# Kernel tuning notes

Measured on AMD Instinct MI355X. Metric: run time of the kernel, lower is better.

Reference implementation:

```python
import jax, jax.numpy as jnp
import numpy as np

LOCAL_SIZE = 128
LN_EPS = 1e-5


def _ln(x):
    # F.layer_norm over last axis, no affine params
    mu = jnp.mean(x, axis=-1, keepdims=True)
    var = jnp.var(x, axis=-1, keepdims=True)
    return (x - mu) / jnp.sqrt(var + LN_EPS)


def _rel_shift(x):
    # x: [b, n, qlen, klen] -> Transformer-XL relative shift
    b, n, q, k = x.shape
    xp = jnp.pad(x, ((0, 0), (0, 0), (0, 0), (1, 0)))
    xp = xp.reshape(b, n, k + 1, q)
    return xp[:, :, 1:, :].reshape(b, n, q, k)


def setup_inputs() -> dict:
    key = jax.random.key(0)
    ks = jax.random.split(key, 12)
    bsz, d_model, qlen, mlen = 16, 1024, 256, 256
    n_head, d_head, d_inner = 16, 64, 4096
    klen = qlen + mlen
    s = 0.02  # param init scale
    return {
        "z1ss": jax.random.normal(ks[0], (bsz, d_model, qlen), jnp.float32),
        "uss": jax.random.normal(ks[1], (bsz, 3 * n_head * d_head, klen), jnp.float32) * 0.1,
        "mems": jax.random.normal(ks[2], (bsz, d_model, mlen), jnp.float32),
        "pos_emb": jax.random.normal(ks[3], (d_model, klen), jnp.float32),
        "Wqkv": jax.random.normal(ks[4], (3 * n_head * d_head, d_model), jnp.float32) * s,
        "Wr": jax.random.normal(ks[5], (n_head * d_head, d_model), jnp.float32) * s,
        "Wo": jax.random.normal(ks[6], (d_model, n_head * d_head), jnp.float32) * s,
        "bo": jnp.zeros((d_model,), jnp.float32),
        "r_w_bias": jax.random.uniform(ks[7], (n_head, d_head), jnp.float32, -0.05, 0.05),
        "r_r_bias": jax.random.uniform(ks[8], (n_head, d_head), jnp.float32, -0.05, 0.05),
        "W1": jax.random.normal(ks[9], (d_inner, d_model), jnp.float32) * s,
        "b1": jnp.zeros((d_inner,), jnp.float32),
        "W2": jax.random.normal(ks[10], (d_model, d_inner), jnp.float32) * s,
        "b2": jnp.zeros((d_model,), jnp.float32),
    }


def reference(z1ss, uss, mems, pos_emb, Wqkv, Wr, Wo, bo, r_w_bias, r_r_bias, W1, b1, W2, b2):
    bsz, d_model, qlen = z1ss.shape
    mlen = mems.shape[-1]
    n_head, d_head = r_w_bias.shape
    scale = 1.0 / (d_head ** 0.5)

    # ---- self-attention with relative positions ----
    cat = jnp.concatenate([mems, z1ss], axis=-1)            # [b, d, klen]
    klen = cat.shape[-1]
    w_heads = jnp.einsum('od,bdk->bok', Wqkv, cat) + uss     # [b, 3*n*dh, klen]
    r_head_k = (Wr @ pos_emb).reshape(n_head, d_head, -1)    # [n, dh, rlen]

    q, k, v = jnp.split(w_heads, 3, axis=1)
    q = q[:, :, -qlen:].reshape(bsz, n_head, d_head, qlen)   # [b, n, dh, q]
    k = k.reshape(bsz, n_head, d_head, klen)
    v = v.reshape(bsz, n_head, d_head, klen)

    AC = jnp.einsum('bndi,bndj->bnij', q + r_w_bias[:, :, None], k)
    BD = jnp.einsum('bndi,ndj->bnij', q + r_r_bias[:, :, None], r_head_k)
    BD = _rel_shift(BD)
    attn_score = (AC + BD) * scale                            # [b, n, q, klen]

    # causal + local-window mask
    i = jnp.arange(qlen)[:, None]
    j = jnp.arange(klen)[None, :]
    mask = (j > i + mlen) | (j <= i + mlen - LOCAL_SIZE)      # [q, klen]
    attn_score = jnp.where(mask[None, None], -1e30, attn_score)

    attn_prob = jax.nn.softmax(attn_score, axis=-1)
    attn_vec = jnp.einsum('bnij,bndj->bndi', attn_prob, v)    # [b, n, dh, q]
    attn_vec = attn_vec.reshape(bsz, n_head * d_head, qlen)
    attn_out = jnp.einsum('od,bdq->boq', Wo, attn_vec) + bo[None, :, None]

    # post-LN residual (pre_lnorm=False), work in [b, q, d]
    h = _ln((attn_out + z1ss).transpose(0, 2, 1))             # [b, q, d]

    # ---- position-wise FF ----
    ff = jax.nn.relu(jnp.einsum('bqd,id->bqi', h, W1) + b1)
    ff = jnp.einsum('bqi,di->bqd', ff, W2) + b2
    out = _ln(ff + h)                                          # [b, q, d]
    return out.transpose(0, 2, 1)                              # [b, d, q]
```

## Files before the change

### kernel.cpp

```cpp
#include <hip/hip_runtime.h>
#include <hip/hip_bf16.h>
#include <math.h>

#define BSZ    16
#define DMODEL 1024
#define QLEN   256
#define MLEN   256
#define KLEN   512
#define NHEAD  16
#define DHEAD  64
#define DINNER 4096

typedef __bf16 bf16;
typedef bf16 bf16x8 __attribute__((ext_vector_type(8)));
typedef float f32x4 __attribute__((ext_vector_type(4)));

#define GLOBAL_AS __attribute__((address_space(1)))
#define LDS_AS    __attribute__((address_space(3)))

__global__ __launch_bounds__(256) void prep_k(
    const float* __restrict__ Wqkv, const float* __restrict__ Wr,
    const float* __restrict__ Wo,   const float* __restrict__ W1,
    const float* __restrict__ W2,   const float* __restrict__ uss,
    const float* __restrict__ mems, const float* __restrict__ z1ss,
    const float* __restrict__ pos_emb,
    bf16* __restrict__ WqkvB, bf16* __restrict__ WrB, bf16* __restrict__ WoB,
    bf16* __restrict__ W1B,   bf16* __restrict__ W2B, bf16* __restrict__ ussV,
    bf16* __restrict__ catT,  bf16* __restrict__ posT,
    bf16* __restrict__ ussQ,  bf16* __restrict__ ussK)
{
    if (blockIdx.x < 21504) {
        long long i = (long long)blockIdx.x * 256 + threadIdx.x;
        const float* src; bf16* dst; long long soff, doff;
        if      (i <  786432) { src = Wqkv; dst = WqkvB; soff = doff = i; }
        else if (i < 1048576) { src = Wr;   dst = WrB;   soff = doff = i -  786432; }
        else if (i < 1310720) { src = Wo;   dst = WoB;   soff = doff = i - 1048576; }
        else if (i < 2359296) { src = W1;   dst = W1B;   soff = doff = i - 1310720; }
        else if (i < 3407872) { src = W2;   dst = W2B;   soff = doff = i - 2359296; }
        else {
            long long u = i - 3407872, b = u >> 17, r = u & 131071;
            src = uss; dst = ussV; soff = b * 393216 + 262144 + r; doff = u;
        }
        float4 v = ((const float4*)src)[soff];
        bf16 b0 = (bf16)v.x, b1 = (bf16)v.y, b2 = (bf16)v.z, b3 = (bf16)v.w;
        union { ushort u[4]; uint2 d; } p;
        p.u[0] = *(ushort*)&b0; p.u[1] = *(ushort*)&b1;
        p.u[2] = *(ushort*)&b2; p.u[3] = *(ushort*)&b3;
        ((uint2*)dst)[doff] = p.d;
        return;
    }
    __shared__ float tile[32][33];
    int blk = blockIdx.x - 21504;
    const float* src; bf16* dst; long long soff, dof; int ld, ldo, tr, tc;
    if (blk < 8192) {
        int bh = blk >> 8, t = blk & 255;
        int b = bh >> 1, half = bh & 1;
        tr = t >> 3; tc = t & 7;
        src = half ? z1ss : mems; soff = (long long)b * 1024 * 256; ld = 256;
        dst = catT; dof = ((long long)b * 512 + half * 256) * 1024; ldo = 1024;
    } else if (blk < 8704) {
        int u = blk - 8192; tr = u >> 4; tc = u & 15;
        src = pos_emb; soff = 0; ld = 512;
        dst = posT; dof = 0; ldo = 1024;
    } else if (blk < 12800) {
        int u = blk - 8704; int b = u >> 8, t = u & 255;
        tr = t >> 3; tc = t & 7;
        src = uss; soff = (long long)b * 3072 * 512 + 256; ld = 512;
        dst = ussQ; dof = (long long)b * 256 * 1024; ldo = 1024;
    } else {
        int u = blk - 12800; int b = u >> 9, t = u & 511;
        tr = t >> 4; tc = t & 15;
        src = uss; soff = ((long long)b * 3072 + 1024) * 512; ld = 512;
        dst = ussK; dof = (long long)b * 512 * 1024; ldo = 1024;
    }
    int tx = threadIdx.x & 31, ty = threadIdx.x >> 5;
    const float* ip = src + soff;
#pragma unroll
    for (int yy = ty; yy < 32; yy += 8)
        tile[yy][tx] = ip[(long long)(tr * 32 + yy) * ld + tc * 32 + tx];
    __syncthreads();
#pragma unroll
    for (int yy = ty; yy < 32; yy += 8)
        dst[dof + (long long)(tc * 32 + yy) * ldo + tr * 32 + tx] = (bf16)tile[tx][yy];
}


__device__ __forceinline__ void stage_a_unit(const bf16* __restrict__ Ag, int ldK,
                                             bf16* sAbuf, int qa, int t) {
    int r  = (t >> 2) & 63;
    int ks = t >> 8;
    int cc = (t & 3) ^ (((t >> 5) & 1) << 1);
    int col = ks * 32 + cc * 8;
    __builtin_amdgcn_global_load_lds(
        (const GLOBAL_AS void*)(Ag + (long long)(qa * 64 + r) * ldK + col),
        (LDS_AS void*)(sAbuf + qa * 4096 + t * 8), 16, 0, 0);
    __builtin_amdgcn_global_load_lds(
        (const GLOBAL_AS void*)(Ag + (long long)(qa * 64 + 128 + r) * ldK + col),
        (LDS_AS void*)(sAbuf + (qa + 2) * 4096 + t * 8), 16, 0, 0);
}

__device__ __forceinline__ void stage_b_unit(const bf16* __restrict__ Bg, int ldK,
                                             bf16* sBbuf, int qb, int t) {
#pragma unroll
    for (int j = 0; j < 2; ++j) {
        int u  = j * 512 + t;
        int p  = u >> 8;
        int w8 = u & 255;
        int ks = w8 >> 7;
        int r  = (w8 >> 2) & 31;
        int cc = (u & 3) ^ (((t >> 5) & 1) << 1);
        __builtin_amdgcn_global_load_lds(
            (const GLOBAL_AS void*)(Bg + (long long)(p * 64 + qb * 32 + r) * ldK + ks * 32 + cc * 8),
            (LDS_AS void*)(sBbuf + p * 4096 + ks * 2048 + qb * 1024 + r * 32 + (u & 3) * 8),
            16, 0, 0);
    }
}

__device__ __forceinline__ void ld_a(const bf16* sAbuf, int qa, int wm, int lane,
                                     bf16x8 a[4][2]) {
    int r16 = lane & 15, qq = lane >> 4;
    int flip = ((r16 >> 3) & 1) << 4;
    const bf16* base = sAbuf + (wm * 2 + qa) * 4096;
#pragma unroll
    for (int mf = 0; mf < 4; ++mf)
#pragma unroll
        for (int ks = 0; ks < 2; ++ks)
            a[mf][ks] = *(const bf16x8*)(base +
                ((ks * 2048 + (mf * 16 + r16) * 32 + qq * 8) ^ flip));
}

__device__ __forceinline__ void ld_b(const bf16* sBbuf, int qb, int wn, int lane,
                                     bf16x8 b[2][2]) {
    int r16 = lane & 15, qq = lane >> 4;
    int flip = ((r16 >> 3) & 1) << 4;
    const bf16* base = sBbuf + wn * 4096 + qb * 1024;
#pragma unroll
    for (int nf = 0; nf < 2; ++nf)
#pragma unroll
        for (int ks = 0; ks < 2; ++ks)
            b[nf][ks] = *(const bf16x8*)(base +
                ((ks * 2048 + (nf * 16 + r16) * 32 + qq * 8) ^ flip));
}

#define PH_SYNC_MFMA(QA, QB)                                                   \
    __builtin_amdgcn_s_barrier();                                              \
    asm volatile("s_waitcnt lgkmcnt(0)" ::: "memory");                         \
    __builtin_amdgcn_s_setprio(1);                                             \
    _Pragma("unroll") for (int ks = 0; ks < 2; ++ks)                           \
    _Pragma("unroll") for (int mf = 0; mf < 4; ++mf)                           \
    _Pragma("unroll") for (int nf = 0; nf < 2; ++nf)                           \
        acc[(QA)*4+mf][(QB)*2+nf] = __builtin_amdgcn_mfma_f32_16x16x32_bf16(   \
            a[mf][ks], b[nf][ks], acc[(QA)*4+mf][(QB)*2+nf], 0, 0, 0);         \
    __builtin_amdgcn_s_setprio(0);                                             \
    __builtin_amdgcn_s_barrier();

__device__ __forceinline__ void gemm8_core(
    const bf16* __restrict__ Ap, const bf16* __restrict__ Bp,
    int ldK, int NT, bf16* sA, bf16* sB, f32x4 (&acc)[8][4])
{
    int t = threadIdx.x;
    int lane = t & 63, w = t >> 6;
    int wm = w >> 2, wn = w & 3;

    stage_a_unit(Ap, ldK, sA, 0, t);
    stage_a_unit(Ap, ldK, sA, 1, t);
    stage_b_unit(Bp, ldK, sB, 0, t);
    stage_b_unit(Bp, ldK, sB, 1, t);
    stage_b_unit(Bp + 64, ldK, sB + 16384, 0, t);
    stage_a_unit(Ap + 64, ldK, sA + 16384, 1, t);
    stage_b_unit(Bp + 64, ldK, sB + 16384, 1, t);
    asm volatile("s_waitcnt vmcnt(6)" ::: "memory");
    __builtin_amdgcn_s_barrier();

    bf16x8 a[4][2], b[2][2];
    for (int g = 0; g < NT; ++g) {
        bf16* AR = sA + (g & 1) * 16384;
        bf16* BR = sB + (g & 1) * 16384;
        bf16* AO = sA + ((g & 1) ^ 1) * 16384;
        const bf16* An = Ap + (long long)(g + 1) * 64;
        const bf16* A2 = Ap + (long long)(g + 2) * 64;
        const bf16* B2 = Bp + (long long)(g + 2) * 64;
        ld_a(AR, 0, wm, lane, a);
        ld_b(BR, 0, wn, lane, b);
        if (g + 1 < NT) stage_a_unit(An, ldK, AO, 0, t);
        PH_SYNC_MFMA(0, 0)
        ld_a(AR, 1, wm, lane, a);
        if (g + 2 < NT) stage_b_unit(B2, ldK, BR, 0, t);
        PH_SYNC_MFMA(1, 0)
        ld_b(BR, 1, wn, lane, b);
        if (g + 2 < NT) stage_a_unit(A2, ldK, AR, 1, t);
        PH_SYNC_MFMA(1, 1)
        ld_a(AR, 0, wm, lane, a);
        if (g + 2 < NT) stage_b_unit(B2, ldK, BR, 1, t);
        if (g < NT - 2) asm volatile("s_waitcnt vmcnt(6)" ::: "memory");
        else            asm volatile("s_waitcnt vmcnt(0)" ::: "memory");
        PH_SYNC_MFMA(0, 1)
    }
}

__global__ __launch_bounds__(512) void qkv8_k(
    const bf16* __restrict__ catT, const bf16* __restrict__ WqkvB,
    const bf16* __restrict__ posT, const bf16* __restrict__ WrB,
    const bf16* __restrict__ ussQ, const bf16* __restrict__ ussK,
    const bf16* __restrict__ ussV,
    bf16* __restrict__ qT, bf16* __restrict__ kT,
    bf16* __restrict__ rhkT, bf16* __restrict__ vB)
{
    __shared__ bf16 sm[65536];
    int f = blockIdx.x;
    int id = (f & 7) * 41 + (f >> 3);

    const bf16 *Ap, *Bp;
    bf16* outp; const bf16* addp;
    long long obase; int ostr;
    if (id < 320) {
        int b = id / 20, rb = id % 20;
        const bf16* cat = catT + (long long)b * 524288;
        if (rb < 4) {
            int n0 = rb << 8;
            Ap = cat + 256 * 1024; Bp = WqkvB + (long long)n0 * 1024;
            outp = qT; addp = ussQ;
            obase = ((long long)b * 256) * 1024 + n0; ostr = 1024;
        } else if (rb < 12) {
            int rr = rb - 4, m0 = (rr >> 2) << 8, n0 = (rr & 3) << 8;
            Ap = cat + (long long)m0 * 1024; Bp = WqkvB + (long long)(1024 + n0) * 1024;
            outp = kT; addp = ussK;
            obase = ((long long)(b * 512 + m0)) * 1024 + n0; ostr = 1024;
        } else {
            int rr = rb - 12, m0 = (rr >> 1) << 8, n0 = (rr & 1) << 8;
            Ap = WqkvB + (long long)(2048 + m0) * 1024; Bp = cat + (long long)n0 * 1024;
            outp = vB; addp = ussV;
            obase = ((long long)(b * 1024 + m0)) * 512 + n0; ostr = 512;
        }
    } else {
        int r = id - 320, m0 = (r >> 2) << 8, n0 = (r & 3) << 8;
        Ap = posT + (long long)m0 * 1024; Bp = WrB + (long long)n0 * 1024;
        outp = rhkT; addp = nullptr;
        obase = (long long)m0 * 1024 + n0; ostr = 1024;
    }

    f32x4 acc[8][4];
#pragma unroll
    for (int i = 0; i < 8; ++i)
#pragma unroll
        for (int j = 0; j < 4; ++j) acc[i][j] = (f32x4){0.f, 0.f, 0.f, 0.f};

    gemm8_core(Ap, Bp, 1024, 16, sm, sm + 32768, acc);

    int t = threadIdx.x, lane = t & 63, w = t >> 6;
    int wm = w >> 2, wn = w & 3;
    int qq = lane >> 4, r16 = lane & 15;
#pragma unroll
    for (int mf = 0; mf < 8; ++mf) {
#pragma unroll
        for (int rr2 = 0; rr2 < 4; ++rr2) {
            int ml = wm * 128 + mf * 16 + qq * 4 + rr2;
#pragma unroll
            for (int nf = 0; nf < 4; ++nf) {
                int nl = wn * 64 + nf * 16 + r16;
                long long idx = obase + (long long)ml * ostr + nl;
                float v = acc[mf][nf][rr2];
                if (addp) v += (float)addp[idx];
                outp[idx] = (bf16)v;
            }
        }
    }
}

__global__ __launch_bounds__(512) void gemm8_k(
    const bf16* __restrict__ A, const bf16* __restrict__ B,
    int N, int K,
    const float* __restrict__ bias, int relu,
    bf16* __restrict__ outB)
{
    __shared__ bf16 sm[65536];
    int nwg = gridDim.x, f = blockIdx.x;
    int xcd = f & 7, l = f >> 3;
    int q8 = nwg >> 3, rm = nwg & 7;
    int wg = (xcd < rm) ? (xcd * (q8 + 1) + l)
                        : (rm * (q8 + 1) + (xcd - rm) * q8 + l);
    int ntn = N >> 8;
    int m0 = (wg / ntn) << 8, n0 = (wg % ntn) << 8;

    f32x4 acc[8][4];
#pragma unroll
    for (int i = 0; i < 8; ++i)
#pragma unroll
        for (int j = 0; j < 4; ++j) acc[i][j] = (f32x4){0.f, 0.f, 0.f, 0.f};

    gemm8_core(A + (long long)m0 * K, B + (long long)n0 * K, K, K >> 6,
               sm, sm + 32768, acc);

    int t = threadIdx.x, lane = t & 63, w = t >> 6;
    int wm = w >> 2, wn = w & 3;
    int qq = lane >> 4, r16 = lane & 15;
#pragma unroll
    for (int mf = 0; mf < 8; ++mf) {
#pragma unroll
        for (int rr2 = 0; rr2 < 4; ++rr2) {
            int m = m0 + wm * 128 + mf * 16 + qq * 4 + rr2;
#pragma unroll
            for (int nf = 0; nf < 4; ++nf) {
                int n = n0 + wn * 64 + nf * 16 + r16;
                float v = acc[mf][nf][rr2];
                if (bias) v += bias[n];
                if (relu) v = fmaxf(v, 0.f);
                outB[(long long)m * N + n] = (bf16)v;
            }
        }
    }
}

__global__ __launch_bounds__(256) void gemm_bf16(
    const bf16* __restrict__ A, const bf16* __restrict__ B,
    int M, int N, int K, int kChunk,
    const float* __restrict__ bias, int relu,
    float* __restrict__ outF, long long ofBatch,
    bf16* __restrict__ outB)
{
    __shared__ bf16 lA[2 * 128 * 32];
    __shared__ bf16 lB[2 * 128 * 32];

    int t = threadIdx.x;
    int w = t >> 6, lane = t & 63;
    int m0 = blockIdx.y * 128, n0 = blockIdx.x * 128;
    int bz = blockIdx.z;

    const bf16* Ap = A;
    const bf16* Bp = B;
    float* oF = outF;
    int Keff = K;
    if (kChunk > 0) {
        Ap = A + (long long)bz * kChunk;
        Bp = B + (long long)bz * kChunk;
        if (outF) oF = outF + (long long)bz * ofBatch;
        Keff = kChunk;
    }

    int q = lane >> 4, r16 = lane & 15;
    int wm = w >> 1, wn = w & 1;

    f32x4 acc[4][4];
#pragma unroll
    for (int i = 0; i < 4; ++i)
#pragma unroll
        for (int j = 0; j < 4; ++j)
            acc[i][j] = (f32x4){0.f, 0.f, 0.f, 0.f};

    int srow = lane >> 2;
    int scol = (lane & 3) * 8;

    for (int k0 = 0; k0 < Keff; k0 += 64) {
        __syncthreads();
#pragma unroll
        for (int half = 0; half < 2; ++half) {
#pragma unroll
            for (int issue = 0; issue < 2; ++issue) {
                int c = issue * 4 + w;
                int row = c * 16 + srow;
                int col = k0 + half * 32 + scol;
                __builtin_amdgcn_global_load_lds(
                    (const GLOBAL_AS void*)(Ap + (long long)(m0 + row) * K + col),
                    (LDS_AS void*)(lA + half * 4096 + c * 512 + lane * 8), 16, 0, 0);
                __builtin_amdgcn_global_load_lds(
                    (const GLOBAL_AS void*)(Bp + (long long)(n0 + row) * K + col),
                    (LDS_AS void*)(lB + half * 4096 + c * 512 + lane * 8), 16, 0, 0);
            }
        }
        __syncthreads();
#pragma unroll
        for (int kh = 0; kh < 2; ++kh) {
            bf16x8 af[4], bfr[4];
#pragma unroll
            for (int i = 0; i < 4; ++i)
                af[i] = *(const bf16x8*)&lA[kh * 4096 + (wm * 64 + i * 16 + r16) * 32 + q * 8];
#pragma unroll
            for (int j = 0; j < 4; ++j)
                bfr[j] = *(const bf16x8*)&lB[kh * 4096 + (wn * 64 + j * 16 + r16) * 32 + q * 8];
#pragma unroll
            for (int i = 0; i < 4; ++i)
#pragma unroll
                for (int j = 0; j < 4; ++j)
                    acc[i][j] = __builtin_amdgcn_mfma_f32_16x16x32_bf16(
                        af[i], bfr[j], acc[i][j], 0, 0, 0);
        }
    }

#pragma unroll
    for (int i = 0; i < 4; ++i) {
#pragma unroll
        for (int r = 0; r < 4; ++r) {
            int m = m0 + wm * 64 + i * 16 + q * 4 + r;
#pragma unroll
            for (int j = 0; j < 4; ++j) {
                int n = n0 + wn * 64 + j * 16 + r16;
                float v = acc[i][j][r];
                if (bias) v += bias[n];
                if (relu) v = fmaxf(v, 0.f);
                if (oF)   oF[(long long)m * N + n] = v;
                if (outB) outB[(long long)m * N + n] = (bf16)v;
            }
        }
    }
}

__global__ __launch_bounds__(256) void attn_mfma_k(
    const bf16* __restrict__ qT,
    const bf16* __restrict__ kT,
    const bf16* __restrict__ vB,
    const bf16* __restrict__ rhkT,
    const float* __restrict__ rwb,
    const float* __restrict__ rrb,
    bf16* __restrict__ avT)
{
    __shared__ float sBD[64][132];

    int t = threadIdx.x;
    int w = t >> 6, lane = t & 63;
    int lo = lane & 15, hi = lane >> 4;
    int i0 = blockIdx.x * 64;
    int n  = blockIdx.y;
    int b  = blockIdx.z;

    const bf16* qp = qT + ((long long)(b * 256 + i0 + 16 * w + lo)) * 1024 + n * 64;
    bf16x8 qw[2], qr[2];
#pragma unroll
    for (int ks = 0; ks < 2; ++ks) {
        bf16x8 qv = *(const bf16x8*)(qp + ks * 32 + hi * 8);
        const float* wb = rwb + n * 64 + ks * 32 + hi * 8;
        const float* rb = rrb + n * 64 + ks * 32 + hi * 8;
#pragma unroll
        for (int e = 0; e < 8; ++e) {
            float qf = (float)qv[e];
            qw[ks][e] = (bf16)(qf + wb[e]);
            qr[ks][e] = (bf16)(qf + rb[e]);
        }
    }

    const bf16* rp = rhkT + (long long)384 * 1024 + n * 64;
#pragma unroll
    for (int tj = 0; tj < 8; ++tj) {
        const bf16* bp = rp + (long long)(16 * tj + lo) * 1024;
        f32x4 a = (f32x4){0.f, 0.f, 0.f, 0.f};
        a = __builtin_amdgcn_mfma_f32_16x16x32_bf16(qr[0], *(const bf16x8*)(bp + hi * 8), a, 0, 0, 0);
        a = __builtin_amdgcn_mfma_f32_16x16x32_bf16(qr[1], *(const bf16x8*)(bp + 32 + hi * 8), a, 0, 0, 0);
#pragma unroll
        for (int r = 0; r < 4; ++r)
            sBD[16 * w + hi * 4 + r][16 * tj + lo] = a[r];
    }
    __syncthreads();

    f32x4 ac[12];
    const bf16* kp = kT + ((long long)b * 512 + i0 + 129) * 1024 + n * 64;
#pragma unroll
    for (int tj = 0; tj < 12; ++tj) {
        const bf16* bp = kp + (long long)(16 * tj + lo) * 1024;
        f32x4 a = (f32x4){0.f, 0.f, 0.f, 0.f};
        a = __builtin_amdgcn_mfma_f32_16x16x32_bf16(qw[0], *(const bf16x8*)(bp + hi * 8), a, 0, 0, 0);
        a = __builtin_amdgcn_mfma_f32_16x16x32_bf16(qw[1], *(const bf16x8*)(bp + 32 + hi * 8), a, 0, 0, 0);
        ac[tj] = a;
    }

    float p[12][4], rowmax[4], rowsum[4];
#pragma unroll
    for (int r = 0; r < 4; ++r) rowmax[r] = -1e30f;
#pragma unroll
    for (int tj = 0; tj < 12; ++tj) {
#pragma unroll
        for (int r = 0; r < 4; ++r) {
            int m = 16 * w + hi * 4 + r;
            int jj = 16 * tj + lo;
            int tt = jj - m;
            float v = (tt >= 0 && tt < 128) ? (ac[tj][r] + sBD[m][tt]) * 0.125f
                                            : -1e30f;
            p[tj][r] = v;
            rowmax[r] = fmaxf(rowmax[r], v);
        }
    }
#pragma unroll
    for (int r = 0; r < 4; ++r) {
        float mx = rowmax[r];
#pragma unroll
        for (int msk = 1; msk < 16; msk <<= 1)
            mx = fmaxf(mx, __shfl_xor(mx, msk, 64));
        rowmax[r] = mx;
        rowsum[r] = 0.f;
    }
#pragma unroll
    for (int tj = 0; tj < 12; ++tj) {
#pragma unroll
        for (int r = 0; r < 4; ++r) {
            float e = exp2f((p[tj][r] - rowmax[r]) * 1.44269504f);
            p[tj][r] = e;
            rowsum[r] += e;
        }
    }
#pragma unroll
    for (int r = 0; r < 4; ++r) {
        float s = rowsum[r];
#pragma unroll
        for (int msk = 1; msk < 16; msk <<= 1)
            s += __shfl_xor(s, msk, 64);
        rowsum[r] = 1.f / s;
    }

    bf16* P = (bf16*)&sBD[0][0];
#pragma unroll
    for (int tj = 0; tj < 12; ++tj) {
#pragma unroll
        for (int r = 0; r < 4; ++r) {
            int m = 16 * w + hi * 4 + r;
            P[m * 264 + 16 * tj + lo] = (bf16)(p[tj][r] * rowsum[r]);
        }
    }
    __syncthreads();

    f32x4 oacc[4];
#pragma unroll
    for (int td = 0; td < 4; ++td) oacc[td] = (f32x4){0.f, 0.f, 0.f, 0.f};
    const bf16* vp = vB + ((long long)b * 1024 + n * 64) * 512 + i0 + 129;
#pragma unroll
    for (int ks = 0; ks < 6; ++ks) {
        bf16x8 af = *(const bf16x8*)(P + (16 * w + lo) * 264 + ks * 32 + hi * 8);
#pragma unroll
        for (int td = 0; td < 4; ++td) {
            bf16x8 bv = *(const bf16x8*)(vp + (long long)(16 * td + lo) * 512 + ks * 32 + hi * 8);
            oacc[td] = __builtin_amdgcn_mfma_f32_16x16x32_bf16(af, bv, oacc[td], 0, 0, 0);
        }
    }
    bf16* op = avT + ((long long)(b * 256 + i0 + 16 * w)) * 1024 + n * 64;
#pragma unroll
    for (int td = 0; td < 4; ++td)
#pragma unroll
        for (int r = 0; r < 4; ++r)
            op[(long long)(hi * 4 + r) * 1024 + 16 * td + lo] = (bf16)oacc[td][r];
}

__global__ __launch_bounds__(256) void ln_bf16_k(
    const float* __restrict__ X1a, const float* __restrict__ X1b,
    const float* __restrict__ bo,  const bf16* __restrict__ catT,
    bf16* __restrict__ H)
{
    int row = blockIdx.x, t = threadIdx.x;
    __shared__ float r1[256], r2[256];
    const float* xa = X1a + (long long)row * 1024;
    const float* xb = X1b + (long long)row * 1024;
    const bf16*  zr = catT + ((long long)(row >> 8) * 512 + 256 + (row & 255)) * 1024;
    float v[4], s = 0.f, ss = 0.f;
#pragma unroll
    for (int u = 0; u < 4; ++u) {
        int c = t + u * 256;
        v[u] = xa[c] + xb[c] + bo[c] + (float)zr[c];
        s += v[u]; ss += v[u] * v[u];
    }
    r1[t] = s; r2[t] = ss;
    __syncthreads();
    for (int off = 128; off > 0; off >>= 1) {
        if (t < off) { r1[t] += r1[t + off]; r2[t] += r2[t + off]; }
        __syncthreads();
    }
    float mean = r1[0] * (1.f / 1024.f);
    float var  = r2[0] * (1.f / 1024.f) - mean * mean;
    float rstd = rsqrtf(var + 1e-5f);
    bf16* hr = H + (long long)row * 1024;
#pragma unroll
    for (int u = 0; u < 4; ++u)
        hr[t + u * 256] = (bf16)((v[u] - mean) * rstd);
}

__global__ __launch_bounds__(256) void ln_final_k(
    const bf16* __restrict__ Hb,
    const float* __restrict__ X2a, const float* __restrict__ X2b,
    const float* __restrict__ b2,
    float* __restrict__ O)
{
    int row = blockIdx.x, t = threadIdx.x;
    int b = row >> 8, qq = row & 255;
    __shared__ float r1[256], r2[256];
    const float* xa = X2a + (long long)row * 1024;
    const float* xb = X2b + (long long)row * 1024;
    const bf16*  hr = Hb  + (long long)row * 1024;

    float y[4], s = 0.f, ss = 0.f;
#pragma unroll
    for (int u = 0; u < 4; ++u) {
        int c = t + u * 256;
        y[u] = xa[c] + xb[c] + b2[c] + (float)hr[c];
        s += y[u]; ss += y[u] * y[u];
    }
    r1[t] = s; r2[t] = ss;
    __syncthreads();
    for (int off = 128; off > 0; off >>= 1) {
        if (t < off) { r1[t] += r1[t + off]; r2[t] += r2[t + off]; }
        __syncthreads();
    }
    float mean = r1[0] * (1.f / 1024.f);
    float var  = r2[0] * (1.f / 1024.f) - mean * mean;
    float rstd = rsqrtf(var + 1e-5f);

    float* ob = O + (long long)b * 1024 * 256 + qq;
#pragma unroll
    for (int u = 0; u < 4; ++u)
        ob[(long long)(t + u * 256) * 256] = (y[u] - mean) * rstd;
}

extern "C" void kernel_launch(void* const* d_in, const int* in_sizes, int n_in,
                              void* d_out, int out_size, void* d_ws, size_t ws_size,
                              hipStream_t stream) {
    const float* z1ss    = (const float*)d_in[0];
    const float* uss     = (const float*)d_in[1];
    const float* mems    = (const float*)d_in[2];
    const float* pos_emb = (const float*)d_in[3];
    const float* Wqkv    = (const float*)d_in[4];
    const float* Wr      = (const float*)d_in[5];
    const float* Wo      = (const float*)d_in[6];
    const float* bo      = (const float*)d_in[7];
    const float* rwb     = (const float*)d_in[8];
    const float* rrb     = (const float*)d_in[9];
    const float* W1      = (const float*)d_in[10];
    const float* b1      = (const float*)d_in[11];
    const float* W2      = (const float*)d_in[12];
    const float* b2      = (const float*)d_in[13];

    char* base = (char*)d_ws;
    bf16*  catT  = (bf16*) (base + 0);
    bf16*  posT  = (bf16*) (base + 16777216);
    bf16*  WqkvB = (bf16*) (base + 17825792);
    bf16*  WrB   = (bf16*) (base + 24117248);
    bf16*  WoB   = (bf16*) (base + 26214400);
    bf16*  W1B   = (bf16*) (base + 28311552);
    bf16*  W2B   = (bf16*) (base + 36700160);
    bf16*  qTB   = (bf16*) (base + 45088768);
    bf16*  kTB   = (bf16*) (base + 53477376);
    bf16*  vBB   = (bf16*) (base + 70254592);
    float* x1a   = (float*)(base + 53477376);
    float* x1b   = (float*)(base + 70254592);
    bf16*  ff_b  = (bf16*) (base + 53477376);
    bf16*  rhkTB = (bf16*) (base + 87031808);
    bf16*  avTB  = (bf16*) (base + 88080384);
    bf16*  ussQb = (bf16*) (base + 96468992);
    bf16*  ussKb = (bf16*) (base + 104857600);
    bf16*  ussVb = (bf16*) (base + 121634816);
    float* x2a   = (float*)(base + 96468992);
    float* x2b   = (float*)(base + 113246208);
    bf16*  hB    = (bf16*) (base + 130023424);

    prep_k<<<42496, 256, 0, stream>>>(
        Wqkv, Wr, Wo, W1, W2, uss, mems, z1ss, pos_emb,
        WqkvB, WrB, WoB, W1B, W2B, ussVb, catT, posT, ussQb, ussKb);

    qkv8_k<<<328, 512, 0, stream>>>(
        catT, WqkvB, posT, WrB, ussQb, ussKb, ussVb, qTB, kTB, rhkTB, vBB);

    attn_mfma_k<<<dim3(4, NHEAD, BSZ), 256, 0, stream>>>(
        qTB, kTB, vBB, rhkTB, rwb, rrb, avTB);

    gemm_bf16<<<dim3(8, 32, 2), 256, 0, stream>>>(
        avTB, WoB, 4096, 1024, 1024, 512,
        nullptr, 0, x1a, (long long)(x1b - x1a), nullptr);

    ln_bf16_k<<<4096, 256, 0, stream>>>(x1a, x1b, bo, catT, hB);

    gemm8_k<<<256, 512, 0, stream>>>(
        hB, W1B, 4096, 1024, b1, 1, ff_b);

    gemm_bf16<<<dim3(8, 32, 2), 256, 0, stream>>>(
        ff_b, W2B, 4096, 1024, 4096, 2048,
        nullptr, 0, x2a, (long long)(x2b - x2a), nullptr);

    ln_final_k<<<4096, 256, 0, stream>>>(hB, x2a, x2b, b2, (float*)d_out);
}
```

Before: 588.6 us.

## Replace QKV kernel with 128-tile GEMM and split-K W2 via gemm8

The 256x256-tile qkv8 kernel is replaced by a simpler 128x128-tile, 256-thread GEMM launched over 1312 workgroups, so more blocks are available to fill the CUs. The second FFN GEMM moves from the older gemm_bf16 kernel to the pipelined gemm8 core with a 4-way split-K. Each split writes its own fp32 partial buffer, and the final LayerNorm sums the four partials. The cost is extra fp32 partial traffic and a qkv GEMM that has no software pipelining across K steps.

```diff
diff --git a/kernel.cpp b/kernel.cpp
--- a/kernel.cpp
+++ b/kernel.cpp
@@ -84,6 +84,114 @@
         dst[dof + (long long)(tc * 32 + yy) * ldo + tr * 32 + tx] = (bf16)tile[tx][yy];
 }
 
+__global__ __launch_bounds__(256) void qkv_gemm_k(
+    const bf16* __restrict__ catT, const bf16* __restrict__ WqkvB,
+    const bf16* __restrict__ posT, const bf16* __restrict__ WrB,
+    const bf16* __restrict__ ussQ, const bf16* __restrict__ ussK,
+    const bf16* __restrict__ ussV,
+    bf16* __restrict__ qT, bf16* __restrict__ kT,
+    bf16* __restrict__ rhkT, bf16* __restrict__ vB)
+{
+    __shared__ bf16 lA[2 * 128 * 32];
+    __shared__ bf16 lB[2 * 128 * 32];
+
+    int f = blockIdx.x;
+    int id = (f & 7) * 164 + (f >> 3);
+    int t = threadIdx.x;
+    int w = t >> 6, lane = t & 63;
+
+    const bf16 *Ap, *Bp;
+    int mode, bz = 0, m0, n0;
+    if (id < 768) {
+        bz = id / 48; int r = id % 48;
+        if (r < 32) { m0 = 256 + ((r >> 4) << 7); n0 = (r & 15) << 7; }
+        else        { int rr = r - 32; m0 = (rr >> 3) << 7; n0 = (8 + (rr & 7)) << 7; }
+        Ap = catT + (long long)bz * 512 * 1024; Bp = WqkvB; mode = 0;
+    } else if (id < 800) {
+        int rr = id - 768; m0 = (rr >> 3) << 7; n0 = (rr & 7) << 7;
+        Ap = posT; Bp = WrB; mode = 1;
+    } else {
+        int rr = id - 800; bz = rr >> 5; int tt = rr & 31;
+        m0 = (tt >> 2) << 7; n0 = (tt & 3) << 7;
+        Ap = WqkvB + 2048 * 1024; Bp = catT + (long long)bz * 512 * 1024; mode = 2;
+    }
+
+    int q = lane >> 4, r16 = lane & 15;
+    int wm = w >> 1, wn = w & 1;
+
+    f32x4 acc[4][4];
+#pragma unroll
+    for (int i = 0; i < 4; ++i)
+#pragma unroll
+        for (int j = 0; j < 4; ++j)
+            acc[i][j] = (f32x4){0.f, 0.f, 0.f, 0.f};
+
+    int srow = lane >> 2;
+    int scol = (lane & 3) * 8;
+
+    for (int k0 = 0; k0 < 1024; k0 += 64) {
+        __syncthreads();
+#pragma unroll
+        for (int half = 0; half < 2; ++half) {
+#pragma unroll
+            for (int issue = 0; issue < 2; ++issue) {
+                int c = issue * 4 + w;
+                int row = c * 16 + srow;
+                int col = k0 + half * 32 + scol;
+                __builtin_amdgcn_global_load_lds(
+                    (const GLOBAL_AS void*)(Ap + (long long)(m0 + row) * 1024 + col),
+                    (LDS_AS void*)(lA + half * 4096 + c * 512 + lane * 8), 16, 0, 0);
+                __builtin_amdgcn_global_load_lds(
+                    (const GLOBAL_AS void*)(Bp + (long long)(n0 + row) * 1024 + col),
+                    (LDS_AS void*)(lB + half * 4096 + c * 512 + lane * 8), 16, 0, 0);
+            }
+        }
+        __syncthreads();
+#pragma unroll
+        for (int kh = 0; kh < 2; ++kh) {
+            bf16x8 af[4], bfr[4];
+#pragma unroll
+            for (int i = 0; i < 4; ++i)
+                af[i] = *(const bf16x8*)&lA[kh * 4096 + (wm * 64 + i * 16 + r16) * 32 + q * 8];
+#pragma unroll
+            for (int j = 0; j < 4; ++j)
+                bfr[j] = *(const bf16x8*)&lB[kh * 4096 + (wn * 64 + j * 16 + r16) * 32 + q * 8];
+#pragma unroll
+            for (int i = 0; i < 4; ++i)
+#pragma unroll
+                for (int j = 0; j < 4; ++j)
+                    acc[i][j] = __builtin_amdgcn_mfma_f32_16x16x32_bf16(
+                        af[i], bfr[j], acc[i][j], 0, 0, 0);
+        }
+    }
+
+    bool isq = (mode == 0) && (n0 < 1024);
+#pragma unroll
+    for (int i = 0; i < 4; ++i) {
+#pragma unroll
+        for (int r = 0; r < 4; ++r) {
+            int m = m0 + wm * 64 + i * 16 + q * 4 + r;
+#pragma unroll
+            for (int j = 0; j < 4; ++j) {
+                int n = n0 + wn * 64 + j * 16 + r16;
+                float v = acc[i][j][r];
+                if (mode == 1) {
+                    rhkT[(long long)m * 1024 + n] = (bf16)v;
+                } else if (mode == 2) {
+                    long long idx = ((long long)bz * 1024 + m) * 512 + n;
+                    vB[idx] = (bf16)(v + (float)ussV[idx]);
+                } else if (isq) {
+                    long long idx = ((long long)(bz * 256 + m - 256) << 10) + n;
+                    qT[idx] = (bf16)(v + (float)ussQ[idx]);
+                } else {
+                    long long idx = ((long long)(bz * 512 + m) << 10) + (n - 1024);
+                    kT[idx] = (bf16)(v + (float)ussK[idx]);
+                }
+            }
+        }
+    }
+}
+
 
 __device__ __forceinline__ void stage_a_unit(const bf16* __restrict__ Ag, int ldK,
                                              bf16* sAbuf, int qa, int t) {
@@ -198,80 +306,12 @@
     }
 }
 
-__global__ __launch_bounds__(512) void qkv8_k(
-    const bf16* __restrict__ catT, const bf16* __restrict__ WqkvB,
-    const bf16* __restrict__ posT, const bf16* __restrict__ WrB,
-    const bf16* __restrict__ ussQ, const bf16* __restrict__ ussK,
-    const bf16* __restrict__ ussV,
-    bf16* __restrict__ qT, bf16* __restrict__ kT,
-    bf16* __restrict__ rhkT, bf16* __restrict__ vB)
-{
-    __shared__ bf16 sm[65536];
-    int f = blockIdx.x;
-    int id = (f & 7) * 41 + (f >> 3);
-
-    const bf16 *Ap, *Bp;
-    bf16* outp; const bf16* addp;
-    long long obase; int ostr;
-    if (id < 320) {
-        int b = id / 20, rb = id % 20;
-        const bf16* cat = catT + (long long)b * 524288;
-        if (rb < 4) {
-            int n0 = rb << 8;
-            Ap = cat + 256 * 1024; Bp = WqkvB + (long long)n0 * 1024;
-            outp = qT; addp = ussQ;
-            obase = ((long long)b * 256) * 1024 + n0; ostr = 1024;
-        } else if (rb < 12) {
-            int rr = rb - 4, m0 = (rr >> 2) << 8, n0 = (rr & 3) << 8;
-            Ap = cat + (long long)m0 * 1024; Bp = WqkvB + (long long)(1024 + n0) * 1024;
-            outp = kT; addp = ussK;
-            obase = ((long long)(b * 512 + m0)) * 1024 + n0; ostr = 1024;
-        } else {
-            int rr = rb - 12, m0 = (rr >> 1) << 8, n0 = (rr & 1) << 8;
-            Ap = WqkvB + (long long)(2048 + m0) * 1024; Bp = cat + (long long)n0 * 1024;
-            outp = vB; addp = ussV;
-            obase = ((long long)(b * 1024 + m0)) * 512 + n0; ostr = 512;
-        }
-    } else {
-        int r = id - 320, m0 = (r >> 2) << 8, n0 = (r & 3) << 8;
-        Ap = posT + (long long)m0 * 1024; Bp = WrB + (long long)n0 * 1024;
-        outp = rhkT; addp = nullptr;
-        obase = (long long)m0 * 1024 + n0; ostr = 1024;
-    }
-
-    f32x4 acc[8][4];
-#pragma unroll
-    for (int i = 0; i < 8; ++i)
-#pragma unroll
-        for (int j = 0; j < 4; ++j) acc[i][j] = (f32x4){0.f, 0.f, 0.f, 0.f};
-
-    gemm8_core(Ap, Bp, 1024, 16, sm, sm + 32768, acc);
-
-    int t = threadIdx.x, lane = t & 63, w = t >> 6;
-    int wm = w >> 2, wn = w & 3;
-    int qq = lane >> 4, r16 = lane & 15;
-#pragma unroll
-    for (int mf = 0; mf < 8; ++mf) {
-#pragma unroll
-        for (int rr2 = 0; rr2 < 4; ++rr2) {
-            int ml = wm * 128 + mf * 16 + qq * 4 + rr2;
-#pragma unroll
-            for (int nf = 0; nf < 4; ++nf) {
-                int nl = wn * 64 + nf * 16 + r16;
-                long long idx = obase + (long long)ml * ostr + nl;
-                float v = acc[mf][nf][rr2];
-                if (addp) v += (float)addp[idx];
-                outp[idx] = (bf16)v;
-            }
-        }
-    }
-}
-
 __global__ __launch_bounds__(512) void gemm8_k(
     const bf16* __restrict__ A, const bf16* __restrict__ B,
-    int N, int K,
+    int N, int K, int kChunk,
     const float* __restrict__ bias, int relu,
-    bf16* __restrict__ outB)
+    bf16* __restrict__ outB,
+    float* __restrict__ outF1, float* __restrict__ outF2)
 {
     __shared__ bf16 sm[65536];
     int nwg = gridDim.x, f = blockIdx.x;
@@ -280,7 +320,19 @@
     int wg = (xcd < rm) ? (xcd * (q8 + 1) + l)
                         : (rm * (q8 + 1) + (xcd - rm) * q8 + l);
     int ntn = N >> 8;
-    int m0 = (wg / ntn) << 8, n0 = (wg % ntn) << 8;
+
+    int Keff = K, split = 0, tile = wg;
+    const bf16* Ap = A;
+    const bf16* Bp = B;
+    if (kChunk > 0) {
+        int nsplit = K / kChunk;
+        int tiles = nwg / nsplit;
+        split = wg / tiles; tile = wg % tiles;
+        Ap += (long long)split * kChunk;
+        Bp += (long long)split * kChunk;
+        Keff = kChunk;
+    }
+    int m0 = (tile / ntn) << 8, n0 = (tile % ntn) << 8;
 
     f32x4 acc[8][4];
 #pragma unroll
@@ -288,24 +340,40 @@
 #pragma unroll
         for (int j = 0; j < 4; ++j) acc[i][j] = (f32x4){0.f, 0.f, 0.f, 0.f};
 
-    gemm8_core(A + (long long)m0 * K, B + (long long)n0 * K, K, K >> 6,
+    gemm8_core(Ap + (long long)m0 * K, Bp + (long long)n0 * K, K, Keff >> 6,
                sm, sm + 32768, acc);
 
     int t = threadIdx.x, lane = t & 63, w = t >> 6;
     int wm = w >> 2, wn = w & 3;
     int qq = lane >> 4, r16 = lane & 15;
-#pragma unroll
-    for (int mf = 0; mf < 8; ++mf) {
-#pragma unroll
-        for (int rr2 = 0; rr2 < 4; ++rr2) {
-            int m = m0 + wm * 128 + mf * 16 + qq * 4 + rr2;
-#pragma unroll
-            for (int nf = 0; nf < 4; ++nf) {
-                int n = n0 + wn * 64 + nf * 16 + r16;
-                float v = acc[mf][nf][rr2];
-                if (bias) v += bias[n];
-                if (relu) v = fmaxf(v, 0.f);
-                outB[(long long)m * N + n] = (bf16)v;
+    if (outB) {
+#pragma unroll
+        for (int mf = 0; mf < 8; ++mf) {
+#pragma unroll
+            for (int rr2 = 0; rr2 < 4; ++rr2) {
+                int m = m0 + wm * 128 + mf * 16 + qq * 4 + rr2;
+#pragma unroll
+                for (int nf = 0; nf < 4; ++nf) {
+                    int n = n0 + wn * 64 + nf * 16 + r16;
+                    float v = acc[mf][nf][rr2];
+                    if (bias) v += bias[n];
+                    if (relu) v = fmaxf(v, 0.f);
+                    outB[(long long)m * N + n] = (bf16)v;
+                }
+            }
+        }
+    } else {
+        float* oF = ((split & 2) ? outF2 : outF1) + (long long)(split & 1) * 4194304;
+#pragma unroll
+        for (int mf = 0; mf < 8; ++mf) {
+#pragma unroll
+            for (int rr2 = 0; rr2 < 4; ++rr2) {
+                int m = m0 + wm * 128 + mf * 16 + qq * 4 + rr2;
+#pragma unroll
+                for (int nf = 0; nf < 4; ++nf) {
+                    int n = n0 + wn * 64 + nf * 16 + r16;
+                    oF[(long long)m * N + n] = acc[mf][nf][rr2];
+                }
             }
         }
     }
@@ -571,6 +639,7 @@
 __global__ __launch_bounds__(256) void ln_final_k(
     const bf16* __restrict__ Hb,
     const float* __restrict__ X2a, const float* __restrict__ X2b,
+    const float* __restrict__ X2c, const float* __restrict__ X2d,
     const float* __restrict__ b2,
     float* __restrict__ O)
 {
@@ -579,13 +648,15 @@
     __shared__ float r1[256], r2[256];
     const float* xa = X2a + (long long)row * 1024;
     const float* xb = X2b + (long long)row * 1024;
+    const float* xc = X2c + (long long)row * 1024;
+    const float* xd = X2d + (long long)row * 1024;
     const bf16*  hr = Hb  + (long long)row * 1024;
 
     float y[4], s = 0.f, ss = 0.f;
 #pragma unroll
     for (int u = 0; u < 4; ++u) {
         int c = t + u * 256;
-        y[u] = xa[c] + xb[c] + b2[c] + (float)hr[c];
+        y[u] = xa[c] + xb[c] + xc[c] + xd[c] + b2[c] + (float)hr[c];
         s += y[u]; ss += y[u] * y[u];
     }
     r1[t] = s; r2[t] = ss;
@@ -643,13 +714,15 @@
     bf16*  ussVb = (bf16*) (base + 121634816);
     float* x2a   = (float*)(base + 96468992);
     float* x2b   = (float*)(base + 113246208);
+    float* x2c   = (float*)(base + 0);
+    float* x2d   = (float*)(base + 16777216);
     bf16*  hB    = (bf16*) (base + 130023424);
 
     prep_k<<<42496, 256, 0, stream>>>(
         Wqkv, Wr, Wo, W1, W2, uss, mems, z1ss, pos_emb,
         WqkvB, WrB, WoB, W1B, W2B, ussVb, catT, posT, ussQb, ussKb);
 
-    qkv8_k<<<328, 512, 0, stream>>>(
+    qkv_gemm_k<<<1312, 256, 0, stream>>>(
         catT, WqkvB, posT, WrB, ussQb, ussKb, ussVb, qTB, kTB, rhkTB, vBB);
 
     attn_mfma_k<<<dim3(4, NHEAD, BSZ), 256, 0, stream>>>(
@@ -662,11 +735,12 @@
     ln_bf16_k<<<4096, 256, 0, stream>>>(x1a, x1b, bo, catT, hB);
 
     gemm8_k<<<256, 512, 0, stream>>>(
-        hB, W1B, 4096, 1024, b1, 1, ff_b);
-
-    gemm_bf16<<<dim3(8, 32, 2), 256, 0, stream>>>(
-        ff_b, W2B, 4096, 1024, 4096, 2048,
-        nullptr, 0, x2a, (long long)(x2b - x2a), nullptr);
-
-    ln_final_k<<<4096, 256, 0, stream>>>(hB, x2a, x2b, b2, (float*)d_out);
-}
+        hB, W1B, 4096, 1024, 0, b1, 1, ff_b, nullptr, nullptr);
+
+    gemm8_k<<<256, 512, 0, stream>>>(
+        ff_b, W2B, 1024, 4096, 1024, nullptr, 0, nullptr,
+        x2c , x2a );
+
+    ln_final_k<<<4096, 256, 0, stream>>>(
+        hB, x2c, x2d, x2a, x2b, b2, (float*)d_out);
+}
```

Measured after the change: 578.6 us. About the same (-1.7%).
